# Kernel optimization log

Hardware: AMD Instinct MI355X
Metric: run time of the kernel (lower is better)

The kernel has to match this reference:

```python
import jax, jax.numpy as jnp
import numpy as np

K = 20
EPS = 1e-5
NEG_SLOPE = 0.2


def knn_idx(x, k):
    # x: (B, C, N) -> idx: (B, N, k) of nearest neighbors by L2 distance
    inner = jnp.einsum('bcn,bcm->bnm', x, x)          # (B, N, N)
    xx = jnp.sum(x * x, axis=1)                        # (B, N)
    # negative squared distance: larger = closer
    neg_dist = 2.0 * inner - xx[:, :, None] - xx[:, None, :]
    _, idx = jax.lax.top_k(neg_dist, k)                # (B, N, k)
    return idx


def edge_feature(x, k):
    # x: (B, C, N) -> (B, 2C, N, k): concat(neighbor - x, x)
    idx = knn_idx(x, k)                                # (B, N, k)
    # neighbors[b,c,n,j] = x[b, c, idx[b,n,j]]
    nbr = jnp.take_along_axis(x[:, :, None, :], idx[:, None, :, :], axis=3)  # (B,C,N,k)
    xc = x[:, :, :, None]
    return jnp.concatenate([nbr - xc, jnp.broadcast_to(xc, nbr.shape)], axis=1)


def conv_bn_lrelu(h, W, gamma, beta):
    # 1x1 conv: h (B, Cin, N, k), W (Cout, Cin)
    h = jnp.einsum('oc,bcnk->bonk', W, h)
    # training-mode BatchNorm2d over (B, N, k) per channel
    mean = jnp.mean(h, axis=(0, 2, 3), keepdims=True)
    var = jnp.var(h, axis=(0, 2, 3), keepdims=True)
    h = (h - mean) * jax.lax.rsqrt(var + EPS)
    h = h * gamma[None, :, None, None] + beta[None, :, None, None]
    return jnp.where(h >= 0, h, NEG_SLOPE * h)


def setup_inputs() -> dict:
    key = jax.random.key(0)
    ks = jax.random.split(key, 3)
    B, C, N = 16, 3, 4096
    x = jax.random.normal(ks[0], (B, C, N), dtype=jnp.float32)
    W0 = jax.random.normal(ks[1], (64, 2 * C), dtype=jnp.float32) * (1.0 / np.sqrt(2 * C))
    W1 = jax.random.normal(ks[2], (64, 64), dtype=jnp.float32) * (1.0 / np.sqrt(64))
    g0 = jnp.ones((64,), jnp.float32); b0 = jnp.zeros((64,), jnp.float32)
    g1 = jnp.ones((64,), jnp.float32); b1 = jnp.zeros((64,), jnp.float32)
    return {"x": x, "W0": W0, "g0": g0, "b0": b0, "W1": W1, "g1": g1, "b1": b1}


def reference(x, W0, g0, b0, W1, g1, b1):
    h = edge_feature(x, K)                 # (B, 2C, N, k)
    h = conv_bn_lrelu(h, W0, g0, b0)       # (B, 64, N, k)
    h = conv_bn_lrelu(h, W1, g1, b1)       # (B, 64, N, k)
    return jnp.max(h, axis=-1)             # (B, 64, N)
```

## Files before the change

kernel.cpp:

```cpp
#include <hip/hip_runtime.h>
#include <cfloat>

#define NEG_SLOPE 0.2f
#define BN_EPS 1e-5f
#define EDGES 1310720
#define INV_M (1.0f / 1310720.0f)

typedef short v8s __attribute__((ext_vector_type(8)));
typedef float v4f __attribute__((ext_vector_type(4)));

__device__ __forceinline__ unsigned short f2bf(float f) {
  unsigned b = __float_as_uint(f);
  b += 0x7fffu + ((b >> 16) & 1u);
  return (unsigned short)(b >> 16);
}
__device__ __forceinline__ float bf2f(unsigned short s) {
  return __uint_as_float(((unsigned)s) << 16);
}

__device__ __forceinline__ float sqnorm_np(float c0, float c1, float c2) {
#pragma clang fp contract(off)
  return (c0 * c0 + c1 * c1) + c2 * c2;
}
__device__ __forceinline__ float negdist_np(float c0, float c1, float c2,
                                            float q0, float q1, float q2,
                                            float xxn, float xxm) {
#pragma clang fp contract(off)
  float inner = (c0 * q0 + c1 * q1) + c2 * q2;
  return (2.0f * inner - xxn) - xxm;
}

__device__ __forceinline__ unsigned orderkey(float f) {
  unsigned u = __float_as_uint(f);
  return ((int)u < 0) ? ~u : (u | 0x80000000u);
}
__device__ __forceinline__ unsigned long long packvi(float v, int m) {
  return ((unsigned long long)orderkey(v) << 32) | (unsigned)(~m);
}

template <int PAT>
__device__ __forceinline__ unsigned long long swz64(unsigned long long v) {
  int hi = __builtin_amdgcn_ds_swizzle((int)(v >> 32), PAT);
  int lo = __builtin_amdgcn_ds_swizzle((int)(unsigned)v, PAT);
  return ((unsigned long long)(unsigned)hi << 32) | (unsigned)lo;
}
__device__ __forceinline__ unsigned long long bperm64(int addr, unsigned long long v) {
  int hi = __builtin_amdgcn_ds_bpermute(addr, (int)(v >> 32));
  int lo = __builtin_amdgcn_ds_bpermute(addr, (int)(unsigned)v);
  return ((unsigned long long)(unsigned)hi << 32) | (unsigned)lo;
}
__device__ __forceinline__ unsigned long long maxu64(unsigned long long a, unsigned long long b) {
  return a > b ? a : b;
}

__device__ __forceinline__ void ins3f(float nd, int m,
                                      float& v0, float& v1, float& v2,
                                      int& i0, int& i1, int& i2) {
  bool g0 = nd > v0, g1 = nd > v1, g2 = nd > v2;
  float nv2 = g2 ? (g1 ? v1 : nd) : v2;  int ni2 = g2 ? (g1 ? i1 : m) : i2;
  float nv1 = g1 ? (g0 ? v0 : nd) : v1;  int ni1 = g1 ? (g0 ? i0 : m) : i1;
  v0 = g0 ? nd : v0;                     i0 = g0 ? m : i0;
  v1 = nv1; i1 = ni1; v2 = nv2; i2 = ni2;
}

__global__ __launch_bounds__(1024, 8) void k1_knn(const float* __restrict__ x, int* __restrict__ idxo) {
  __shared__ float xs0[4096], xs1[4096], xs2[4096], xs3[4096];
  int b   = blockIdx.x >> 5;
  int blk = blockIdx.x & 31;
  const float* xb = x + b * 12288;
  for (int i = threadIdx.x; i < 4096; i += 1024) {
    float a0 = xb[i], a1 = xb[4096 + i], a2 = xb[8192 + i];
    xs0[i] = a0; xs1[i] = a1; xs2[i] = a2;
    xs3[i] = sqnorm_np(a0, a1, a2);
  }
  __syncthreads();

  int wv = threadIdx.x >> 6;
  int lane = threadIdx.x & 63;
  int wave_id = blk * 16 + wv;
  int xaddr = ((lane ^ 32) << 2);

  #pragma unroll 1
  for (int p = 0; p < 4; p++) {
    int nA = wave_id * 8 + 2 * p;
    int nB = nA + 1;
    float qA0 = xs0[nA], qA1 = xs1[nA], qA2 = xs2[nA];
    float qB0 = xs0[nB], qB1 = xs1[nB], qB2 = xs2[nB];
    float xxnA = xs3[nA];
    float xxnB = xs3[nB];

    float vA0 = -FLT_MAX, vA1 = -FLT_MAX, vA2 = -FLT_MAX;
    float vB0 = -FLT_MAX, vB1 = -FLT_MAX, vB2 = -FLT_MAX;
    int   iA0 = 0x7fffffff, iA1 = 0x7fffffff, iA2 = 0x7fffffff;
    int   iB0 = 0x7fffffff, iB1 = 0x7fffffff, iB2 = 0x7fffffff;
    #pragma unroll 2
    for (int j = 0; j < 64; j++) {
      int m = (j << 6) + lane;
      float c0 = xs0[m], c1 = xs1[m], c2 = xs2[m];
      float xxm = xs3[m];
      float ndA = negdist_np(c0, c1, c2, qA0, qA1, qA2, xxnA, xxm);
      ins3f(ndA, m, vA0, vA1, vA2, iA0, iA1, iA2);
      float ndB = negdist_np(c0, c1, c2, qB0, qB1, qB2, xxnB, xxm);
      ins3f(ndB, m, vB0, vB1, vB2, iB0, iB1, iB2);
    }

    unsigned long long remA = 0ull, remB = 0ull;
    int keepA = 0, keepB = 0;
    #pragma unroll 1
    for (int r = 0; r < 20; r++) {
      unsigned long long wA = packvi(vA0, iA0);
      unsigned long long wB = packvi(vB0, iB0);
      wA = maxu64(wA, swz64<0x041F>(wA)); wB = maxu64(wB, swz64<0x041F>(wB));
      wA = maxu64(wA, swz64<0x081F>(wA)); wB = maxu64(wB, swz64<0x081F>(wB));
      wA = maxu64(wA, swz64<0x101F>(wA)); wB = maxu64(wB, swz64<0x101F>(wB));
      wA = maxu64(wA, swz64<0x201F>(wA)); wB = maxu64(wB, swz64<0x201F>(wB));
      wA = maxu64(wA, swz64<0x401F>(wA)); wB = maxu64(wB, swz64<0x401F>(wB));
      wA = maxu64(wA, bperm64(xaddr, wA)); wB = maxu64(wB, bperm64(xaddr, wB));

      int mA = (int)~(unsigned)wA;
      int mB = (int)~(unsigned)wB;
      if (lane == r) { keepA = mA; keepB = mB; }

      bool ownA = ((mA & 63) == lane);
      remA |= ownA ? (1ull << (mA >> 6)) : 0ull;
      vA0 = ownA ? vA1 : vA0;  iA0 = ownA ? iA1 : iA0;
      vA1 = ownA ? vA2 : vA1;  iA1 = ownA ? iA2 : iA1;
      vA2 = ownA ? -FLT_MAX : vA2;  iA2 = ownA ? 0x7fffffff : iA2;
      if (ownA & (vA0 == -FLT_MAX)) {
        #pragma unroll 1
        for (int j = 0; j < 64; j++) {
          int m = (j << 6) + lane;
          float c0 = xs0[m], c1 = xs1[m], c2 = xs2[m];
          float xxm = xs3[m];
          float ndA = negdist_np(c0, c1, c2, qA0, qA1, qA2, xxnA, xxm);
          if ((remA >> j) & 1ull) ndA = -FLT_MAX;
          ins3f(ndA, m, vA0, vA1, vA2, iA0, iA1, iA2);
        }
      }
      bool ownB = ((mB & 63) == lane);
      remB |= ownB ? (1ull << (mB >> 6)) : 0ull;
      vB0 = ownB ? vB1 : vB0;  iB0 = ownB ? iB1 : iB0;
      vB1 = ownB ? vB2 : vB1;  iB1 = ownB ? iB2 : iB1;
      vB2 = ownB ? -FLT_MAX : vB2;  iB2 = ownB ? 0x7fffffff : iB2;
      if (ownB & (vB0 == -FLT_MAX)) {
        #pragma unroll 1
        for (int j = 0; j < 64; j++) {
          int m = (j << 6) + lane;
          float c0 = xs0[m], c1 = xs1[m], c2 = xs2[m];
          float xxm = xs3[m];
          float ndB = negdist_np(c0, c1, c2, qB0, qB1, qB2, xxnB, xxm);
          if ((remB >> j) & 1ull) ndB = -FLT_MAX;
          ins3f(ndB, m, vB0, vB1, vB2, iB0, iB1, iB2);
        }
      }
    }
    if (lane < 20) {
      idxo[((b << 12) + nA) * 20 + lane] = keepA;
      idxo[((b << 12) + nB) * 20 + lane] = keepB;
    }
  }
}

__global__ __launch_bounds__(256) void k2_moments(const float* __restrict__ x,
                                                  const int* __restrict__ idxi,
                                                  float* __restrict__ stat) {
  float acc[27];
  #pragma unroll
  for (int i = 0; i < 27; i++) acc[i] = 0.f;
  int stride = gridDim.x * blockDim.x;
  for (int e = blockIdx.x * blockDim.x + threadIdx.x; e < EDGES; e += stride) {
    int P = e / 20;
    int b = P >> 12;
    int n = P & 4095;
    int m = idxi[e];
    const float* xb = x + b * 12288;
    float xn0 = xb[n], xn1 = xb[4096 + n], xn2 = xb[8192 + n];
    float ev[6];
    ev[0] = xb[m] - xn0; ev[1] = xb[4096 + m] - xn1; ev[2] = xb[8192 + m] - xn2;
    ev[3] = xn0; ev[4] = xn1; ev[5] = xn2;
    int p = 6;
    #pragma unroll
    for (int i2 = 0; i2 < 6; i2++) {
      acc[i2] += ev[i2];
      #pragma unroll
      for (int j2 = i2; j2 < 6; j2++) { acc[p] = fmaf(ev[i2], ev[j2], acc[p]); p++; }
    }
  }
  #pragma unroll
  for (int i = 0; i < 27; i++) {
    float s = acc[i];
    for (int off = 32; off > 0; off >>= 1) s += __shfl_down(s, off);
    acc[i] = s;
  }
  __shared__ float red[4][27];
  int w = threadIdx.x >> 6, lane = threadIdx.x & 63;
  if (lane == 0) {
    #pragma unroll
    for (int i = 0; i < 27; i++) red[w][i] = acc[i];
  }
  __syncthreads();
  if (threadIdx.x < 27) {
    float s = red[0][threadIdx.x] + red[1][threadIdx.x] + red[2][threadIdx.x] + red[3][threadIdx.x];
    atomicAdd(&stat[threadIdx.x], s);
  }
}

__global__ void k3_fin1(const float* __restrict__ stat, const float* __restrict__ W0,
                        const float* __restrict__ g0, const float* __restrict__ b0,
                        float* __restrict__ a1o, float* __restrict__ b1o) {
  int c = threadIdx.x;
  float w[6];
  #pragma unroll
  for (int i = 0; i < 6; i++) w[i] = W0[c * 6 + i];
  float mean = 0.f;
  #pragma unroll
  for (int i = 0; i < 6; i++) mean += w[i] * stat[i];
  mean *= INV_M;
  float e2 = 0.f;
  int p = 6;
  #pragma unroll
  for (int i = 0; i < 6; i++) {
    #pragma unroll
    for (int j = i; j < 6; j++) {
      float f = w[i] * w[j] * stat[p]; p++;
      e2 += (i == j) ? f : 2.f * f;
    }
  }
  e2 *= INV_M;
  float var = e2 - mean * mean;
  float a = g0[c] * rsqrtf(var + BN_EPS);
  a1o[c] = a;
  b1o[c] = b0[c] - mean * a;
}

__global__ __launch_bounds__(256) void k0_uv(const float* __restrict__ x, const float* __restrict__ W0,
                                             const float* __restrict__ a1, const float* __restrict__ b1e,
                                             unsigned short* __restrict__ u, unsigned short* __restrict__ v) {
  int gid = blockIdx.x * 256 + threadIdx.x;
  int p = gid >> 6;
  int c = gid & 63;
  int b = p >> 12, n = p & 4095;
  const float* xb = x + b * 12288;
  float x0 = xb[n], x1 = xb[4096 + n], x2 = xb[8192 + n];
  float w0 = W0[c * 6], w1 = W0[c * 6 + 1], w2 = W0[c * 6 + 2];
  float w3 = W0[c * 6 + 3], w4 = W0[c * 6 + 4], w5 = W0[c * 6 + 5];
  float a = a1[c], bb = b1e[c];
  float uu = a * (w0 * x0 + w1 * x1 + w2 * x2);
  float vv = a * ((w3 - w0) * x0 + (w4 - w1) * x1 + (w5 - w2) * x2) + bb;
  u[gid] = f2bf(uu);
  v[gid] = f2bf(vv);
}

__global__ __launch_bounds__(256, 4) void k4_mfma(const unsigned short* __restrict__ u,
                                                  const unsigned short* __restrict__ v,
                                                  const int* __restrict__ idxi,
                                                  const float* __restrict__ W1,
                                                  float* __restrict__ psum,
                                                  unsigned short* __restrict__ maxb,
                                                  unsigned short* __restrict__ minb) {
  int lane = threadIdx.x & 63;
  int wv = threadIdx.x >> 6;
  int g = blockIdx.x * 4 + wv;
  int G = g * 16;
  int bbase = (G >> 12) << 12;
  int row16 = lane & 15;
  int quad = lane >> 4;

  v8s Bf[4][2];
  #pragma unroll
  for (int t = 0; t < 4; t++) {
    const float* wrow = W1 + (16 * t + row16) * 64 + quad * 8;
    #pragma unroll
    for (int kh = 0; kh < 2; kh++) {
      #pragma unroll
      for (int i = 0; i < 8; i++) Bf[t][kh][i] = (short)f2bf(wrow[kh * 32 + i]);
    }
  }
  const v8s* vrow = (const v8s*)(v + (G + row16) * 64);
  v8s vv0 = vrow[quad], vv1 = vrow[quad + 4];
  float v0f[8], v1f[8];
  #pragma unroll
  for (int i = 0; i < 8; i++) {
    v0f[i] = bf2f((unsigned short)vv0[i]);
    v1f[i] = bf2f((unsigned short)vv1[i]);
  }

  const int* ip = idxi + (G + row16) * 20;

  float mx[4][4], mn[4][4], s2a[4], sq2a[4];
  #pragma unroll
  for (int t = 0; t < 4; t++) {
    #pragma unroll
    for (int i = 0; i < 4; i++) { mx[t][i] = -FLT_MAX; mn[t][i] = FLT_MAX; }
    s2a[t] = 0.f; sq2a[t] = 0.f;
  }

  int m_next = ip[0];
  #pragma unroll 1
  for (int j = 0; j < 20; j++) {
    int m = bbase + m_next;
    if (j < 19) m_next = ip[j + 1];
    const v8s* urow = (const v8s*)(u + m * 64);
    v8s u0 = urow[quad], u1 = urow[quad + 4];
    v8s a0, a1f;
    #pragma unroll
    for (int i = 0; i < 8; i++) {
      float h = bf2f((unsigned short)u0[i]) + v0f[i];
      h = fmaxf(h, 0.2f * h);
      a0[i] = (short)f2bf(h);
      float h2 = bf2f((unsigned short)u1[i]) + v1f[i];
      h2 = fmaxf(h2, 0.2f * h2);
      a1f[i] = (short)f2bf(h2);
    }
    #pragma unroll
    for (int t = 0; t < 4; t++) {
      v4f c = {0.f, 0.f, 0.f, 0.f};
      c = __builtin_amdgcn_mfma_f32_16x16x32_bf16(a0, Bf[t][0], c, 0, 0, 0);
      c = __builtin_amdgcn_mfma_f32_16x16x32_bf16(a1f, Bf[t][1], c, 0, 0, 0);
      #pragma unroll
      for (int i = 0; i < 4; i++) {
        float cv = c[i];
        mx[t][i] = fmaxf(mx[t][i], cv);
        mn[t][i] = fminf(mn[t][i], cv);
        s2a[t] += cv;
        sq2a[t] = fmaf(cv, cv, sq2a[t]);
      }
    }
  }
  #pragma unroll
  for (int t = 0; t < 4; t++) {
    #pragma unroll
    for (int i = 0; i < 4; i++) {
      int P = G + quad * 4 + i;
      maxb[P * 64 + 16 * t + row16] = f2bf(mx[t][i]);
      minb[P * 64 + 16 * t + row16] = f2bf(mn[t][i]);
    }
  }
  #pragma unroll
  for (int t = 0; t < 4; t++) {
    float s = s2a[t], q = sq2a[t];
    s += __shfl_xor(s, 16); q += __shfl_xor(q, 16);
    s += __shfl_xor(s, 32); q += __shfl_xor(q, 32);
    if (quad == 0) {
      int c = 16 * t + row16;
      psum[c * 4096 + g] = s;
      psum[(64 + c) * 4096 + g] = q;
    }
  }
}

__global__ __launch_bounds__(256) void k4b_red(const float* __restrict__ psum, float* __restrict__ s2) {
  int c = blockIdx.x;
  const float* p = psum + c * 4096;
  float s = 0.f;
  for (int i = threadIdx.x; i < 4096; i += 256) s += p[i];
  for (int off = 32; off > 0; off >>= 1) s += __shfl_down(s, off);
  __shared__ float red[4];
  if ((threadIdx.x & 63) == 0) red[threadIdx.x >> 6] = s;
  __syncthreads();
  if (threadIdx.x == 0) s2[c] = red[0] + red[1] + red[2] + red[3];
}

__global__ __launch_bounds__(256) void k5_out(const unsigned short* __restrict__ maxb,
                                              const unsigned short* __restrict__ minb,
                                              const float* __restrict__ s2, const float* __restrict__ g1,
                                              const float* __restrict__ b1, float* __restrict__ out) {
  __shared__ float T[64][65];
  __shared__ float a2s[64], b2s[64];
  int blk = blockIdx.x;
  int b = blk >> 6;
  int n0 = (blk & 63) << 6;
  int t = threadIdx.x;
  if (t < 64) {
    float mean = s2[t] * INV_M;
    float var = s2[64 + t] * INV_M - mean * mean;
    float a = g1[t] * rsqrtf(var + BN_EPS);
    a2s[t] = a;
    b2s[t] = b1[t] - mean * a;
  }
  __syncthreads();
  #pragma unroll
  for (int i = 0; i < 16; i++) {
    int lin = i * 256 + t;
    int r = lin >> 6;
    int c = lin & 63;
    float a = a2s[c];
    int P = (b << 12) + n0 + r;
    float vfp = bf2f((a >= 0.f) ? maxb[P * 64 + c] : minb[P * 64 + c]);
    float z = a * vfp + b2s[c];
    T[c][r] = z >= 0.f ? z : NEG_SLOPE * z;
  }
  __syncthreads();
  #pragma unroll
  for (int i = 0; i < 16; i++) {
    int lin = i * 256 + t;
    int c = lin >> 6;
    int nn = lin & 63;
    out[(b * 64 + c) * 4096 + n0 + nn] = T[c][nn];
  }
}

extern "C" void kernel_launch(void* const* d_in, const int* in_sizes, int n_in,
                              void* d_out, int out_size, void* d_ws, size_t ws_size,
                              hipStream_t stream) {
  const float* x  = (const float*)d_in[0];
  const float* W0 = (const float*)d_in[1];
  const float* g0 = (const float*)d_in[2];
  const float* b0 = (const float*)d_in[3];
  const float* W1 = (const float*)d_in[4];
  const float* g1 = (const float*)d_in[5];
  const float* b1 = (const float*)d_in[6];
  float* out = (float*)d_out;
  char* ws = (char*)d_ws;

  int*            idx  = (int*)(ws + 0);
  float*          stat = (float*)(ws + 5242880);
  float*          a1   = (float*)(ws + 5242880 + 512);
  float*          b1e  = (float*)(ws + 5242880 + 768);
  float*          s2   = (float*)(ws + 5242880 + 1024);
  float*          part = (float*)(ws + 5244416);
  unsigned short* u    = (unsigned short*)(ws + 7341568);
  unsigned short* v    = (unsigned short*)(ws + 15730176);
  unsigned short* maxb = (unsigned short*)(ws + 24118784);
  unsigned short* minb = (unsigned short*)(ws + 32507392);

  (void)hipMemsetAsync(stat, 0, 128, stream);
  k1_knn    <<<512, 1024, 0, stream>>>(x, idx);
  k2_moments<<<1024, 256, 0, stream>>>(x, idx, stat);
  k3_fin1   <<<1, 64, 0, stream>>>(stat, W0, g0, b0, a1, b1e);
  k0_uv     <<<16384, 256, 0, stream>>>(x, W0, a1, b1e, u, v);
  k4_mfma   <<<1024, 256, 0, stream>>>(u, v, idx, W1, part, maxb, minb);
  k4b_red   <<<128, 256, 0, stream>>>(part, s2);
  k5_out    <<<1024, 256, 0, stream>>>(maxb, minb, s2, g1, b1, out);
}
```

Baseline: 454.0 us.

## Pack kNN shared data as float4, process four queries per wave, restructure moments

The kNN kernel now stores x and its squared norm interleaved as float4 in shared memory and handles four query points per pass instead of two, so each candidate load is reused across more queries and LDS instructions are reduced. The moments kernel is rewritten so each thread owns one point, loops over its 20 neighbors and derives the cross terms with the centre point algebraically, avoiding a per-edge division and redundant center loads. It launches 256 blocks instead of 1024, one thread per point. Register pressure rises in kNN with four top-3 lists per lane, and the float accumulation order in the moments changes slightly.

```diff
diff --git a/kernel.cpp b/kernel.cpp
--- a/kernel.cpp
+++ b/kernel.cpp
@@ -64,14 +64,13 @@
 }
 
 __global__ __launch_bounds__(1024, 8) void k1_knn(const float* __restrict__ x, int* __restrict__ idxo) {
-  __shared__ float xs0[4096], xs1[4096], xs2[4096], xs3[4096];
+  __shared__ float4 xs[4096];
   int b   = blockIdx.x >> 5;
   int blk = blockIdx.x & 31;
   const float* xb = x + b * 12288;
   for (int i = threadIdx.x; i < 4096; i += 1024) {
     float a0 = xb[i], a1 = xb[4096 + i], a2 = xb[8192 + i];
-    xs0[i] = a0; xs1[i] = a1; xs2[i] = a2;
-    xs3[i] = sqnorm_np(a0, a1, a2);
+    xs[i] = make_float4(a0, a1, a2, sqnorm_np(a0, a1, a2));
   }
   __syncthreads();
 
@@ -81,82 +80,76 @@
   int xaddr = ((lane ^ 32) << 2);
 
   #pragma unroll 1
-  for (int p = 0; p < 4; p++) {
-    int nA = wave_id * 8 + 2 * p;
-    int nB = nA + 1;
-    float qA0 = xs0[nA], qA1 = xs1[nA], qA2 = xs2[nA];
-    float qB0 = xs0[nB], qB1 = xs1[nB], qB2 = xs2[nB];
-    float xxnA = xs3[nA];
-    float xxnB = xs3[nB];
-
-    float vA0 = -FLT_MAX, vA1 = -FLT_MAX, vA2 = -FLT_MAX;
-    float vB0 = -FLT_MAX, vB1 = -FLT_MAX, vB2 = -FLT_MAX;
-    int   iA0 = 0x7fffffff, iA1 = 0x7fffffff, iA2 = 0x7fffffff;
-    int   iB0 = 0x7fffffff, iB1 = 0x7fffffff, iB2 = 0x7fffffff;
+  for (int pp = 0; pp < 2; pp++) {
+    int nQ = wave_id * 8 + 4 * pp;
+    float4 q[4];
+    #pragma unroll
+    for (int qq = 0; qq < 4; qq++) q[qq] = xs[nQ + qq];
+
+    float v0[4], v1[4], v2[4];
+    int   i0[4], i1[4], i2[4];
+    #pragma unroll
+    for (int qq = 0; qq < 4; qq++) {
+      v0[qq] = v1[qq] = v2[qq] = -FLT_MAX;
+      i0[qq] = i1[qq] = i2[qq] = 0x7fffffff;
+    }
     #pragma unroll 2
     for (int j = 0; j < 64; j++) {
       int m = (j << 6) + lane;
-      float c0 = xs0[m], c1 = xs1[m], c2 = xs2[m];
-      float xxm = xs3[m];
-      float ndA = negdist_np(c0, c1, c2, qA0, qA1, qA2, xxnA, xxm);
-      ins3f(ndA, m, vA0, vA1, vA2, iA0, iA1, iA2);
-      float ndB = negdist_np(c0, c1, c2, qB0, qB1, qB2, xxnB, xxm);
-      ins3f(ndB, m, vB0, vB1, vB2, iB0, iB1, iB2);
-    }
-
-    unsigned long long remA = 0ull, remB = 0ull;
-    int keepA = 0, keepB = 0;
+      float4 c = xs[m];
+      #pragma unroll
+      for (int qq = 0; qq < 4; qq++) {
+        float nd = negdist_np(c.x, c.y, c.z, q[qq].x, q[qq].y, q[qq].z, q[qq].w, c.w);
+        ins3f(nd, m, v0[qq], v1[qq], v2[qq], i0[qq], i1[qq], i2[qq]);
+      }
+    }
+
+    unsigned long long rem[4] = {0ull, 0ull, 0ull, 0ull};
+    int keep[4] = {0, 0, 0, 0};
     #pragma unroll 1
     for (int r = 0; r < 20; r++) {
-      unsigned long long wA = packvi(vA0, iA0);
-      unsigned long long wB = packvi(vB0, iB0);
-      wA = maxu64(wA, swz64<0x041F>(wA)); wB = maxu64(wB, swz64<0x041F>(wB));
-      wA = maxu64(wA, swz64<0x081F>(wA)); wB = maxu64(wB, swz64<0x081F>(wB));
-      wA = maxu64(wA, swz64<0x101F>(wA)); wB = maxu64(wB, swz64<0x101F>(wB));
-      wA = maxu64(wA, swz64<0x201F>(wA)); wB = maxu64(wB, swz64<0x201F>(wB));
-      wA = maxu64(wA, swz64<0x401F>(wA)); wB = maxu64(wB, swz64<0x401F>(wB));
-      wA = maxu64(wA, bperm64(xaddr, wA)); wB = maxu64(wB, bperm64(xaddr, wB));
-
-      int mA = (int)~(unsigned)wA;
-      int mB = (int)~(unsigned)wB;
-      if (lane == r) { keepA = mA; keepB = mB; }
-
-      bool ownA = ((mA & 63) == lane);
-      remA |= ownA ? (1ull << (mA >> 6)) : 0ull;
-      vA0 = ownA ? vA1 : vA0;  iA0 = ownA ? iA1 : iA0;
-      vA1 = ownA ? vA2 : vA1;  iA1 = ownA ? iA2 : iA1;
-      vA2 = ownA ? -FLT_MAX : vA2;  iA2 = ownA ? 0x7fffffff : iA2;
-      if (ownA & (vA0 == -FLT_MAX)) {
-        #pragma unroll 1
-        for (int j = 0; j < 64; j++) {
-          int m = (j << 6) + lane;
-          float c0 = xs0[m], c1 = xs1[m], c2 = xs2[m];
-          float xxm = xs3[m];
-          float ndA = negdist_np(c0, c1, c2, qA0, qA1, qA2, xxnA, xxm);
-          if ((remA >> j) & 1ull) ndA = -FLT_MAX;
-          ins3f(ndA, m, vA0, vA1, vA2, iA0, iA1, iA2);
+      unsigned long long w[4];
+      #pragma unroll
+      for (int qq = 0; qq < 4; qq++) w[qq] = packvi(v0[qq], i0[qq]);
+      #pragma unroll
+      for (int qq = 0; qq < 4; qq++) w[qq] = maxu64(w[qq], swz64<0x041F>(w[qq]));
+      #pragma unroll
+      for (int qq = 0; qq < 4; qq++) w[qq] = maxu64(w[qq], swz64<0x081F>(w[qq]));
+      #pragma unroll
+      for (int qq = 0; qq < 4; qq++) w[qq] = maxu64(w[qq], swz64<0x101F>(w[qq]));
+      #pragma unroll
+      for (int qq = 0; qq < 4; qq++) w[qq] = maxu64(w[qq], swz64<0x201F>(w[qq]));
+      #pragma unroll
+      for (int qq = 0; qq < 4; qq++) w[qq] = maxu64(w[qq], swz64<0x401F>(w[qq]));
+      #pragma unroll
+      for (int qq = 0; qq < 4; qq++) w[qq] = maxu64(w[qq], bperm64(xaddr, w[qq]));
+
+      #pragma unroll
+      for (int qq = 0; qq < 4; qq++) {
+        int mw = (int)~(unsigned)w[qq];
+        if (lane == r) keep[qq] = mw;
+        bool own = ((mw & 63) == lane);
+        rem[qq] |= own ? (1ull << (mw >> 6)) : 0ull;
+        v0[qq] = own ? v1[qq] : v0[qq];  i0[qq] = own ? i1[qq] : i0[qq];
+        v1[qq] = own ? v2[qq] : v1[qq];  i1[qq] = own ? i2[qq] : i1[qq];
+        v2[qq] = own ? -FLT_MAX : v2[qq];  i2[qq] = own ? 0x7fffffff : i2[qq];
+        if (own & (v0[qq] == -FLT_MAX)) {
+          float4 qx = xs[nQ + qq];
+          #pragma unroll 1
+          for (int j = 0; j < 64; j++) {
+            int m = (j << 6) + lane;
+            float4 c = xs[m];
+            float nd = negdist_np(c.x, c.y, c.z, qx.x, qx.y, qx.z, qx.w, c.w);
+            if ((rem[qq] >> j) & 1ull) nd = -FLT_MAX;
+            ins3f(nd, m, v0[qq], v1[qq], v2[qq], i0[qq], i1[qq], i2[qq]);
+          }
         }
       }
-      bool ownB = ((mB & 63) == lane);
-      remB |= ownB ? (1ull << (mB >> 6)) : 0ull;
-      vB0 = ownB ? vB1 : vB0;  iB0 = ownB ? iB1 : iB0;
-      vB1 = ownB ? vB2 : vB1;  iB1 = ownB ? iB2 : iB1;
-      vB2 = ownB ? -FLT_MAX : vB2;  iB2 = ownB ? 0x7fffffff : iB2;
-      if (ownB & (vB0 == -FLT_MAX)) {
-        #pragma unroll 1
-        for (int j = 0; j < 64; j++) {
-          int m = (j << 6) + lane;
-          float c0 = xs0[m], c1 = xs1[m], c2 = xs2[m];
-          float xxm = xs3[m];
-          float ndB = negdist_np(c0, c1, c2, qB0, qB1, qB2, xxnB, xxm);
-          if ((remB >> j) & 1ull) ndB = -FLT_MAX;
-          ins3f(ndB, m, vB0, vB1, vB2, iB0, iB1, iB2);
-        }
-      }
     }
     if (lane < 20) {
-      idxo[((b << 12) + nA) * 20 + lane] = keepA;
-      idxo[((b << 12) + nB) * 20 + lane] = keepB;
+      #pragma unroll
+      for (int qq = 0; qq < 4; qq++)
+        idxo[((b << 12) + nQ + qq) * 20 + lane] = keep[qq];
     }
   }
 }
@@ -164,28 +157,33 @@
 __global__ __launch_bounds__(256) void k2_moments(const float* __restrict__ x,
                                                   const int* __restrict__ idxi,
                                                   float* __restrict__ stat) {
+  int P = blockIdx.x * 256 + threadIdx.x;
+  int b = P >> 12, n = P & 4095;
+  const float* xb = x + b * 12288;
+  float xn0 = xb[n], xn1 = xb[4096 + n], xn2 = xb[8192 + n];
+  const int* ip = idxi + P * 20;
+  float Sd0 = 0.f, Sd1 = 0.f, Sd2 = 0.f;
+  float S00 = 0.f, S01 = 0.f, S02 = 0.f, S11 = 0.f, S12 = 0.f, S22 = 0.f;
+  #pragma unroll 4
+  for (int j = 0; j < 20; j++) {
+    int m = ip[j];
+    float d0 = xb[m] - xn0, d1 = xb[4096 + m] - xn1, d2 = xb[8192 + m] - xn2;
+    Sd0 += d0; Sd1 += d1; Sd2 += d2;
+    S00 = fmaf(d0, d0, S00); S01 = fmaf(d0, d1, S01); S02 = fmaf(d0, d2, S02);
+    S11 = fmaf(d1, d1, S11); S12 = fmaf(d1, d2, S12); S22 = fmaf(d2, d2, S22);
+  }
   float acc[27];
-  #pragma unroll
-  for (int i = 0; i < 27; i++) acc[i] = 0.f;
-  int stride = gridDim.x * blockDim.x;
-  for (int e = blockIdx.x * blockDim.x + threadIdx.x; e < EDGES; e += stride) {
-    int P = e / 20;
-    int b = P >> 12;
-    int n = P & 4095;
-    int m = idxi[e];
-    const float* xb = x + b * 12288;
-    float xn0 = xb[n], xn1 = xb[4096 + n], xn2 = xb[8192 + n];
-    float ev[6];
-    ev[0] = xb[m] - xn0; ev[1] = xb[4096 + m] - xn1; ev[2] = xb[8192 + m] - xn2;
-    ev[3] = xn0; ev[4] = xn1; ev[5] = xn2;
-    int p = 6;
-    #pragma unroll
-    for (int i2 = 0; i2 < 6; i2++) {
-      acc[i2] += ev[i2];
-      #pragma unroll
-      for (int j2 = i2; j2 < 6; j2++) { acc[p] = fmaf(ev[i2], ev[j2], acc[p]); p++; }
-    }
-  }
+  acc[0] = Sd0; acc[1] = Sd1; acc[2] = Sd2;
+  acc[3] = 20.f * xn0; acc[4] = 20.f * xn1; acc[5] = 20.f * xn2;
+  acc[6] = S00;  acc[7] = S01;  acc[8] = S02;
+  acc[9] = Sd0 * xn0;  acc[10] = Sd0 * xn1; acc[11] = Sd0 * xn2;
+  acc[12] = S11; acc[13] = S12;
+  acc[14] = Sd1 * xn0; acc[15] = Sd1 * xn1; acc[16] = Sd1 * xn2;
+  acc[17] = S22;
+  acc[18] = Sd2 * xn0; acc[19] = Sd2 * xn1; acc[20] = Sd2 * xn2;
+  acc[21] = 20.f * xn0 * xn0; acc[22] = 20.f * xn0 * xn1; acc[23] = 20.f * xn0 * xn2;
+  acc[24] = 20.f * xn1 * xn1; acc[25] = 20.f * xn1 * xn2;
+  acc[26] = 20.f * xn2 * xn2;
   #pragma unroll
   for (int i = 0; i < 27; i++) {
     float s = acc[i];
@@ -426,7 +424,7 @@
 
   (void)hipMemsetAsync(stat, 0, 128, stream);
   k1_knn    <<<512, 1024, 0, stream>>>(x, idx);
-  k2_moments<<<1024, 256, 0, stream>>>(x, idx, stat);
+  k2_moments<<<256, 256, 0, stream>>>(x, idx, stat);
   k3_fin1   <<<1, 64, 0, stream>>>(stat, W0, g0, b0, a1, b1e);
   k0_uv     <<<16384, 256, 0, stream>>>(x, W0, a1, b1e, u, v);
   k4_mfma   <<<1024, 256, 0, stream>>>(u, v, idx, W1, part, maxb, minb);
```

New measurement: 463.2 us. 1.02x slower.
